# Optimization experiments

Measured on AMD Instinct MI355X. Metric: run time of the kernel, lower is better.

## Reference

```python
import jax, jax.numpy as jnp
import numpy as np

B, N, K = 32, 1024, 20

def _knn_idx(x, k):
    # x: [B, N, C] -> indices of k nearest neighbors (excluding self): [B, N, k]
    sq = jnp.sum(x * x, axis=-1)                      # [B, N]
    d = sq[:, :, None] + sq[:, None, :] - 2.0 * jnp.einsum('bnc,bmc->bnm', x, x)
    d = jnp.where(jnp.eye(x.shape[1], dtype=bool)[None], jnp.inf, d)
    _, idx = jax.lax.top_k(-d, k)                     # smallest distances
    return idx

def _edge_conv(x, k, mlp):
    # x: [B, N, C]; dynamic kNN graph + nn(cat[x_i, x_j - x_i]) + max over neighbors
    idx = _knn_idx(x, k)                              # [B, N, k]
    xj = jax.vmap(lambda xb, ib: xb[ib])(x, idx)      # [B, N, k, C]
    xi = jnp.broadcast_to(x[:, :, None, :], xj.shape)
    msg = mlp(jnp.concatenate([xi, xj - xi], axis=-1))  # [B, N, k, H]
    return jnp.max(msg, axis=2)                       # [B, N, H]

def setup_inputs() -> dict:
    key = jax.random.key(0)
    ks = jax.random.split(key, 16)
    def lin(kk, fi, fo):
        return jax.random.normal(kk, (fi, fo), dtype=jnp.float32) / np.sqrt(fi)
    x = jax.random.normal(ks[0], (B * N, 3), dtype=jnp.float32)
    batch = jnp.repeat(jnp.arange(B, dtype=jnp.int64), N)
    return {
        'x': x, 'batch': batch,
        'W1': lin(ks[1], 6, 64),   'b1': jnp.zeros((64,), jnp.float32),
        'W2': lin(ks[2], 64, 64),  'b2': jnp.zeros((64,), jnp.float32),
        'W3': lin(ks[3], 64, 64),  'b3': jnp.zeros((64,), jnp.float32),
        'W4': lin(ks[4], 128, 128),'b4': jnp.zeros((128,), jnp.float32),
        'Wp': lin(ks[5], 128, 512),'bp': jnp.zeros((512,), jnp.float32),
        'Wt1': lin(ks[6], 512, 256),'bt1': jnp.zeros((256,), jnp.float32),
        'Wt2': lin(ks[7], 256, 40), 'bt2': jnp.zeros((40,), jnp.float32),
    }

def reference(x, batch, W1, b1, W2, b2, W3, b3, W4, b4, Wp, bp, Wt1, bt1, Wt2, bt2):
    xb = x.reshape(B, N, -1)  # equal-sized clouds per batch vector
    mlp1 = lambda h: jax.nn.relu(jax.nn.relu(jax.nn.relu(h @ W1 + b1) @ W2 + b2) @ W3 + b3)
    mlp2 = lambda h: jax.nn.relu(h @ W4 + b4)
    out = _edge_conv(xb, K, mlp1)          # [B, N, 64]
    out = _edge_conv(out, K, mlp2)         # [B, N, 128]
    out = jax.nn.relu(out @ Wp + bp)       # [B, N, 512]
    out = jnp.max(out, axis=1)             # global max pool -> [B, 512]
    out = jax.nn.relu(out @ Wt1 + bt1) @ Wt2 + bt2  # [B, 40]
    return out
```

## Files before the change

kernel.cpp:

```cpp
#include <hip/hip_runtime.h>
#include <math.h>

#define BN   1024
#define NB   32
#define KNN  20
#define NROWS (NB*BN)

typedef __attribute__((ext_vector_type(8))) short bf16x8_t;
typedef __attribute__((ext_vector_type(4))) float f32x4_t;

__device__ __forceinline__ float finf() { return __builtin_huge_valf(); }

__device__ __forceinline__ unsigned short f2bf(float f) {
  union { float f; unsigned u; } v; v.f = f;
  unsigned r = v.u + 0x7FFFu + ((v.u >> 16) & 1u);
  return (unsigned short)(r >> 16);
}
__device__ __forceinline__ float bf2f(unsigned short h) {
  union { unsigned u; float f; } v; v.u = ((unsigned)h) << 16; return v.f;
}

__device__ __forceinline__ unsigned fkey(float d) {
  union { float f; unsigned u; } v; v.f = d;
  return (v.u & 0x80000000u) ? ~v.u : (v.u | 0x80000000u);
}

__device__ __forceinline__ void emit20(const unsigned (&kq)[16], unsigned thr,
                                       int lane, unsigned short* __restrict__ idx_out) {
  const unsigned long long lmask = (1ull << lane) - 1ull;
  int base = 0;
#pragma unroll
  for (int t = 0; t < 16; ++t) {
    const bool ok = (kq[t] <= thr);
    const unsigned long long m = __ballot(ok);
    if (ok) idx_out[base + (int)__popcll(m & lmask)] = (unsigned short)(kq[t] & 1023u);
    base += (int)__popcll(m);
  }
}

__device__ __forceinline__ void emit20c(const unsigned (&kq)[16], unsigned P, int cnt_lt,
                                        int lane, unsigned short* __restrict__ idx_out) {
  const unsigned long long lmask = (1ull << lane) - 1ull;
  const int need = KNN - cnt_lt;
  int base_lt = 0, base_eq = 0;
#pragma unroll
  for (int t = 0; t < 16; ++t) {
    const bool lt = (kq[t] < P);
    const bool eq = ((kq[t] - P) < 1024u);
    const unsigned long long mlt = __ballot(lt);
    const unsigned long long meq = __ballot(eq);
    if (lt) idx_out[base_lt + (int)__popcll(mlt & lmask)] = (unsigned short)(kq[t] & 1023u);
    const int erank = base_eq + (int)__popcll(meq & lmask);
    if (eq && erank < need) idx_out[cnt_lt + erank] = (unsigned short)(kq[t] & 1023u);
    base_lt += (int)__popcll(mlt);
    base_eq += (int)__popcll(meq);
  }
}

__device__ __forceinline__ void select20x2(const unsigned (&k0)[16], const unsigned (&k1)[16],
    int lane, unsigned short* __restrict__ o0, unsigned short* __restrict__ o1) {
  unsigned p0 = 0u, p1 = 0u;
  bool d0 = false, d1 = false;
#pragma unroll 1
  for (int b = 31; b >= 10; --b) {
    if (!d0) {
      const unsigned cand = p0 | (1u << b);
      int cnt = 0;
#pragma unroll
      for (int t = 0; t < 16; ++t) cnt += (int)__popcll(__ballot(k0[t] < cand));
      if (cnt == KNN)      { p0 = cand - 1u; d0 = true; }
      else if (cnt < KNN)  { p0 = cand; }
    }
    if (!d1) {
      const unsigned cand = p1 | (1u << b);
      int cnt = 0;
#pragma unroll
      for (int t = 0; t < 16; ++t) cnt += (int)__popcll(__ballot(k1[t] < cand));
      if (cnt == KNN)      { p1 = cand - 1u; d1 = true; }
      else if (cnt < KNN)  { p1 = cand; }
    }
    if (d0 && d1) break;
  }
  if (d0) emit20(k0, p0, lane, o0);
  else {
    int c = 0;
#pragma unroll
    for (int t = 0; t < 16; ++t) c += (int)__popcll(__ballot(k0[t] < p0));
    emit20c(k0, p0, c, lane, o0);
  }
  if (d1) emit20(k1, p1, lane, o1);
  else {
    int c = 0;
#pragma unroll
    for (int t = 0; t < 16; ++t) c += (int)__popcll(__ballot(k1[t] < p1));
    emit20c(k1, p1, c, lane, o1);
  }
}

__global__ __launch_bounds__(256) void prep_kernel(const float* __restrict__ W2, const float* __restrict__ W3,
    const float* __restrict__ W4, const float* __restrict__ Wp,
    unsigned short* __restrict__ w2b, unsigned short* __restrict__ w3b,
    unsigned short* __restrict__ w4b, unsigned short* __restrict__ wpb) {
  const int i = blockIdx.x * 256 + threadIdx.x;
  if (i < 512) {
    const int lane = i & 63, ks = (i >> 6) & 1, nt = i >> 7;
    const int col = nt*16 + (lane & 15), k0 = ks*32 + ((lane >> 4) << 3);
#pragma unroll
    for (int e = 0; e < 8; ++e) w2b[i*8 + e] = f2bf(W2[(size_t)(k0 + e)*64 + col]);
  } else if (i < 1024) {
    const int ii = i - 512;
    const int lane = ii & 63, ks = (ii >> 6) & 1, nt = ii >> 7;
    const int col = nt*16 + (lane & 15), k0 = ks*32 + ((lane >> 4) << 3);
#pragma unroll
    for (int e = 0; e < 8; ++e) w3b[ii*8 + e] = f2bf(W3[(size_t)(k0 + e)*64 + col]);
  } else if (i < 3072) {
    const int ii = i - 1024;
    const int lane = ii & 63, ks = (ii >> 6) & 3, nt = ii >> 8;
    const int col = nt*16 + (lane & 15), k0 = ks*32 + ((lane >> 4) << 3);
#pragma unroll
    for (int e = 0; e < 8; ++e) w4b[ii*8 + e] = f2bf(W4[(size_t)(k0 + e)*128 + col]);
  } else if (i < 11264) {
    const int ii = i - 3072;
    const int lane = ii & 63, ks = (ii >> 6) & 3, nt = ii >> 8;
    const int col = nt*16 + (lane & 15), k0 = ks*32 + ((lane >> 4) << 3);
#pragma unroll
    for (int e = 0; e < 8; ++e) {
      const float v = Wp[(size_t)(k0 + e)*512 + col];
      const unsigned short h = f2bf(v);
      wpb[ii*8 + e]         = h;
      wpb[65536 + ii*8 + e] = f2bf(v - bf2f(h));
    }
  }
}

__global__ __launch_bounds__(256) void knn3_kernel(const float* __restrict__ x, unsigned short* __restrict__ idxo) {
  const int pair = blockIdx.x * 4 + (threadIdx.x >> 6);
  const int lane = threadIdx.x & 63;
  const int row0 = pair * 2;
  const int b = row0 >> 10;
  const int ia = row0 & (BN - 1), ib = ia + 1;
  const float* xb = x + (size_t)b * BN * 3;
  const float xa0 = xb[ia*3+0], xa1 = xb[ia*3+1], xa2 = xb[ia*3+2];
  const float xb0 = xb[ib*3+0], xb1 = xb[ib*3+1], xb2 = xb[ib*3+2];
  const float sqa = xa0*xa0 + xa1*xa1 + xa2*xa2;
  const float sqb = xb0*xb0 + xb1*xb1 + xb2*xb2;
  unsigned k0[16], k1[16];
#pragma unroll
  for (int t = 0; t < 16; ++t) {
    const int j = (t << 6) | lane;
    const float a0 = xb[j*3+0], a1 = xb[j*3+1], a2 = xb[j*3+2];
    const float sqj = a0*a0 + a1*a1 + a2*a2;
    const float da  = sqa + sqj - 2.0f*(xa0*a0 + xa1*a1 + xa2*a2);
    const float db  = sqb + sqj - 2.0f*(xb0*a0 + xb1*a1 + xb2*a2);
    k0[t] = (j == ia) ? 0xFFFFFFFFu : ((fkey(da) & 0xFFFFFC00u) | (unsigned)j);
    k1[t] = (j == ib) ? 0xFFFFFFFFu : ((fkey(db) & 0xFFFFFC00u) | (unsigned)j);
  }
  select20x2(k0, k1, lane, idxo + (size_t)row0 * KNN, idxo + (size_t)(row0 + 1) * KNN);
}

__global__ __launch_bounds__(256) void edge1_mfma_kernel(const float* __restrict__ x, const unsigned short* __restrict__ idx,
    const float* __restrict__ W1, const float* __restrict__ B1,
    const unsigned short* __restrict__ w2b, const float* __restrict__ B2,
    const unsigned short* __restrict__ w3b, const float* __restrict__ B3,
    float* __restrict__ out1, unsigned short* __restrict__ hib,
    unsigned short* __restrict__ lob, float* __restrict__ sqbuf) {
  __shared__ unsigned short Hs1[80*64];
  __shared__ unsigned short Hs2[80*64];
  __shared__ float part[4][4];
  const int t = threadIdx.x, lane = t & 63, w = t >> 6;
  const int node0 = blockIdx.x * 4;

  const int bcol = w*16 + (lane & 15);
  bf16x8_t Bf2[2], Bf3[2];
#pragma unroll
  for (int ks = 0; ks < 2; ++ks) {
    Bf2[ks] = *(const bf16x8_t*)&w2b[(size_t)((w*2 + ks)*64 + lane) * 8];
    Bf3[ks] = *(const bf16x8_t*)&w3b[(size_t)((w*2 + ks)*64 + lane) * 8];
  }

  float w1c[6];
#pragma unroll
  for (int c = 0; c < 6; ++c) w1c[c] = W1[c*64 + lane];
  const float b1o = B1[lane];
  for (int r = w; r < 80; r += 4) {
    const int g = (r * 205) >> 12;
    const int e = r - g*20;
    const int node = node0 + g;
    const int b = node >> 10;
    const int j = idx[(size_t)node*KNN + e];
    const float xi0 = x[(size_t)node*3+0], xi1 = x[(size_t)node*3+1], xi2 = x[(size_t)node*3+2];
    const size_t jr = ((size_t)(b*BN + j))*3;
    const float h3 = x[jr+0]-xi0, h4 = x[jr+1]-xi1, h5 = x[jr+2]-xi2;
    float z = b1o + xi0*w1c[0] + xi1*w1c[1] + xi2*w1c[2]
                  + h3*w1c[3] + h4*w1c[4] + h5*w1c[5];
    z = fmaxf(z, 0.0f);
    Hs1[r*64 + (((lane>>3) ^ (r&7))<<3) + (lane&7)] = f2bf(z);
  }
  __syncthreads();

  f32x4_t acc[5];
#pragma unroll
  for (int mt = 0; mt < 5; ++mt) acc[mt] = (f32x4_t){0,0,0,0};
#pragma unroll
  for (int ks = 0; ks < 2; ++ks) {
#pragma unroll
    for (int mt = 0; mt < 5; ++mt) {
      const int r = mt*16 + (lane & 15);
      const int chunk = ks*4 + (lane >> 4);
      const bf16x8_t a = *(const bf16x8_t*)&Hs1[r*64 + ((chunk ^ (r&7))<<3)];
      acc[mt] = __builtin_amdgcn_mfma_f32_16x16x32_bf16(a, Bf2[ks], acc[mt], 0,0,0);
    }
  }
  {
    const float b2o = B2[bcol];
    const int rbase = (lane >> 4) * 4;
#pragma unroll
    for (int mt = 0; mt < 5; ++mt) {
#pragma unroll
      for (int reg = 0; reg < 4; ++reg) {
        const int row = mt*16 + rbase + reg;
        const float v = fmaxf(acc[mt][reg] + b2o, 0.0f);
        Hs2[row*64 + (((bcol>>3) ^ (row&7))<<3) + (bcol&7)] = f2bf(v);
      }
    }
  }
  __syncthreads();

#pragma unroll
  for (int mt = 0; mt < 5; ++mt) acc[mt] = (f32x4_t){0,0,0,0};
#pragma unroll
  for (int ks = 0; ks < 2; ++ks) {
#pragma unroll
    for (int mt = 0; mt < 5; ++mt) {
      const int r = mt*16 + (lane & 15);
      const int chunk = ks*4 + (lane >> 4);
      const bf16x8_t a = *(const bf16x8_t*)&Hs2[r*64 + ((chunk ^ (r&7))<<3)];
      acc[mt] = __builtin_amdgcn_mfma_f32_16x16x32_bf16(a, Bf3[ks], acc[mt], 0,0,0);
    }
  }

  {
    const float b3o = B3[bcol];
    const int rbase = (lane >> 4) * 4;
    float nm0 = 0.0f, nm1 = 0.0f, nm2 = 0.0f, nm3 = 0.0f;
#pragma unroll
    for (int mt = 0; mt < 5; ++mt) {
#pragma unroll
      for (int reg = 0; reg < 4; ++reg) {
        const int r = mt*16 + rbase + reg;
        const int g = (r * 205) >> 12;
        const float v = fmaxf(acc[mt][reg] + b3o, 0.0f);
        nm0 = (g == 0) ? fmaxf(nm0, v) : nm0;
        nm1 = (g == 1) ? fmaxf(nm1, v) : nm1;
        nm2 = (g == 2) ? fmaxf(nm2, v) : nm2;
        nm3 = (g == 3) ? fmaxf(nm3, v) : nm3;
      }
    }
#pragma unroll
    for (int off = 16; off <= 32; off <<= 1) {
      nm0 = fmaxf(nm0, __shfl_xor(nm0, off, 64));
      nm1 = fmaxf(nm1, __shfl_xor(nm1, off, 64));
      nm2 = fmaxf(nm2, __shfl_xor(nm2, off, 64));
      nm3 = fmaxf(nm3, __shfl_xor(nm3, off, 64));
    }
    const int gq = lane >> 4;
    const float m = (gq == 0) ? nm0 : (gq == 1) ? nm1 : (gq == 2) ? nm2 : nm3;
    const int node = node0 + gq;
    out1[(size_t)node*64 + bcol] = m;
    const unsigned short h = f2bf(m);
    hib[(size_t)node*64 + bcol] = h;
    lob[(size_t)node*64 + bcol] = f2bf(m - bf2f(h));
    float s = m * m;
#pragma unroll
    for (int off = 1; off <= 8; off <<= 1) s += __shfl_xor(s, off, 64);
    if ((lane & 15) == 0) part[gq][w] = s;
  }
  __syncthreads();
  if (t < 4) sqbuf[node0 + t] = part[t][0] + part[t][1] + part[t][2] + part[t][3];
}

__global__ __launch_bounds__(512) void knn64_mfma_kernel(
    const unsigned short* __restrict__ hi, const unsigned short* __restrict__ lo,
    const float* __restrict__ sq, unsigned short* __restrict__ idxo) {
  __shared__ unsigned Dmat[16 * 1024];
  const int t = threadIdx.x, lane = t & 63, w = t >> 6;
  const int i0  = blockIdx.x * 16;
  const int b   = i0 >> 10;
  const int i0l = i0 & (BN - 1);

  const size_t arow = (size_t)(i0 + (lane & 15)) * 64;
  const int    koff = (lane >> 4) * 8;
  bf16x8_t Ahi[2], Alo[2];
#pragma unroll
  for (int ks = 0; ks < 2; ++ks) {
    Ahi[ks] = *(const bf16x8_t*)&hi[arow + ks*32 + koff];
    Alo[ks] = *(const bf16x8_t*)&lo[arow + ks*32 + koff];
  }

  f32x4_t acc[8];
#pragma unroll
  for (int nt = 0; nt < 8; ++nt) {
    const int jl = (8*w + nt)*16 + (lane & 15);
    const size_t jrow = ((size_t)(b << 10) + jl) * 64;
    const bf16x8_t Bhi0 = *(const bf16x8_t*)&hi[jrow + koff];
    const bf16x8_t Bhi1 = *(const bf16x8_t*)&hi[jrow + 32 + koff];
    const bf16x8_t Blo0 = *(const bf16x8_t*)&lo[jrow + koff];
    const bf16x8_t Blo1 = *(const bf16x8_t*)&lo[jrow + 32 + koff];
    f32x4_t a = (f32x4_t){0,0,0,0};
    a = __builtin_amdgcn_mfma_f32_16x16x32_bf16(Ahi[0], Bhi0, a, 0,0,0);
    a = __builtin_amdgcn_mfma_f32_16x16x32_bf16(Ahi[1], Bhi1, a, 0,0,0);
    a = __builtin_amdgcn_mfma_f32_16x16x32_bf16(Ahi[0], Blo0, a, 0,0,0);
    a = __builtin_amdgcn_mfma_f32_16x16x32_bf16(Ahi[1], Blo1, a, 0,0,0);
    a = __builtin_amdgcn_mfma_f32_16x16x32_bf16(Alo[0], Bhi0, a, 0,0,0);
    a = __builtin_amdgcn_mfma_f32_16x16x32_bf16(Alo[1], Bhi1, a, 0,0,0);
    acc[nt] = a;
  }

  const int rbase = (lane >> 4) * 4;
  float sqr[4];
#pragma unroll
  for (int r = 0; r < 4; ++r) sqr[r] = sq[i0 + rbase + r];
#pragma unroll
  for (int nt = 0; nt < 8; ++nt) {
    const int jl = (8*w + nt)*16 + (lane & 15);
    const float sqj = sq[(b << 10) + jl];
#pragma unroll
    for (int r = 0; r < 4; ++r) {
      const float d = sqr[r] + sqj - 2.0f * acc[nt][r];
      const unsigned kq = (jl == i0l + rbase + r) ? 0xFFFFFFFFu
                        : ((fkey(d) & 0xFFFFFC00u) | (unsigned)jl);
      Dmat[(rbase + r)*1024 + jl] = kq;
    }
  }
  __syncthreads();

  const int r0 = 2*w, r1 = 2*w + 1;
  unsigned k0[16], k1[16];
#pragma unroll
  for (int tt = 0; tt < 16; ++tt) {
    k0[tt] = Dmat[r0*1024 + tt*64 + lane];
    k1[tt] = Dmat[r1*1024 + tt*64 + lane];
  }
  select20x2(k0, k1, lane, idxo + (size_t)(i0 + r0) * KNN, idxo + (size_t)(i0 + r1) * KNN);
}

__global__ __launch_bounds__(256) void edge2_mfma_kernel(const float* __restrict__ f, const unsigned short* __restrict__ idx,
    const unsigned short* __restrict__ w4b, const float* __restrict__ B4,
    unsigned short* __restrict__ o2hi, unsigned short* __restrict__ o2lo) {
  __shared__ unsigned short Hs[160*128];
  const int t = threadIdx.x, lane = t & 63, w = t >> 6;
  const int node0 = blockIdx.x * 8;

  bf16x8_t Bfrag[2][4];
#pragma unroll
  for (int nti = 0; nti < 2; ++nti)
#pragma unroll
    for (int ks = 0; ks < 4; ++ks)
      Bfrag[nti][ks] = *(const bf16x8_t*)&w4b[(size_t)(((2*w + nti)*4 + ks)*64 + lane) * 8];

  const int cq = (lane & 15) * 4;
  const int ch1 = cq >> 3, ch2 = 8 + (cq >> 3), sub = cq & 4;
#pragma unroll 2
  for (int i = 0; i < 10; ++i) {
    const int r = w*40 + i*4 + (lane >> 4);
    const int g = (r * 205) >> 12;
    const int e = r - g*20;
    const int node = node0 + g;
    const int b = node >> 10;
    const int j = idx[(size_t)node*KNN + e];
    const float4 xi = *(const float4*)&f[(size_t)node*64 + cq];
    const float4 xj = *(const float4*)&f[((size_t)(b*BN + j))*64 + cq];
    ushort4 hxi, hdf;
    hxi.x = f2bf(xi.x); hxi.y = f2bf(xi.y); hxi.z = f2bf(xi.z); hxi.w = f2bf(xi.w);
    hdf.x = f2bf(xj.x - xi.x); hdf.y = f2bf(xj.y - xi.y);
    hdf.z = f2bf(xj.z - xi.z); hdf.w = f2bf(xj.w - xi.w);
    *(ushort4*)&Hs[r*128 + ((ch1 ^ (r&7))<<3) + sub] = hxi;
    *(ushort4*)&Hs[r*128 + ((ch2 ^ (r&7))<<3) + sub] = hdf;
  }
  __syncthreads();

  f32x4_t acc[10][2];
#pragma unroll
  for (int mt = 0; mt < 10; ++mt) { acc[mt][0] = (f32x4_t){0,0,0,0}; acc[mt][1] = (f32x4_t){0,0,0,0}; }
#pragma unroll
  for (int ks = 0; ks < 4; ++ks) {
#pragma unroll
    for (int mt = 0; mt < 10; ++mt) {
      const int r = mt*16 + (lane & 15);
      const int chunk = ks*4 + (lane >> 4);
      const bf16x8_t a = *(const bf16x8_t*)&Hs[r*128 + ((chunk ^ (r&7))<<3)];
      acc[mt][0] = __builtin_amdgcn_mfma_f32_16x16x32_bf16(a, Bfrag[0][ks], acc[mt][0], 0,0,0);
      acc[mt][1] = __builtin_amdgcn_mfma_f32_16x16x32_bf16(a, Bfrag[1][ks], acc[mt][1], 0,0,0);
    }
  }

  const float bb0 = B4[(2*w+0)*16 + (lane & 15)];
  const float bb1 = B4[(2*w+1)*16 + (lane & 15)];
  const int rbase = (lane >> 4) * 4;
  float nm[8][2];
#pragma unroll
  for (int g = 0; g < 8; ++g) { nm[g][0] = 0.0f; nm[g][1] = 0.0f; }
#pragma unroll
  for (int mt = 0; mt < 10; ++mt) {
#pragma unroll
    for (int reg = 0; reg < 4; ++reg) {
      const int base = mt*16 + reg;
      const int glo = base / 20, ghi = (base + 12) / 20;
      const int r = base + rbase;
      const float v0 = fmaxf(acc[mt][0][reg] + bb0, 0.0f);
      const float v1 = fmaxf(acc[mt][1][reg] + bb1, 0.0f);
      if (glo == ghi) {
        nm[glo][0] = fmaxf(nm[glo][0], v0);
        nm[glo][1] = fmaxf(nm[glo][1], v1);
      } else {
        const bool hi = (r >= ghi*20);
        nm[glo][0] = hi ? nm[glo][0] : fmaxf(nm[glo][0], v0);
        nm[glo][1] = hi ? nm[glo][1] : fmaxf(nm[glo][1], v1);
        nm[ghi][0] = hi ? fmaxf(nm[ghi][0], v0) : nm[ghi][0];
        nm[ghi][1] = hi ? fmaxf(nm[ghi][1], v1) : nm[ghi][1];
      }
    }
  }
#pragma unroll
  for (int off = 16; off <= 32; off <<= 1)
#pragma unroll
    for (int g = 0; g < 8; ++g) {
      nm[g][0] = fmaxf(nm[g][0], __shfl_xor(nm[g][0], off, 64));
      nm[g][1] = fmaxf(nm[g][1], __shfl_xor(nm[g][1], off, 64));
    }
  const int gq = lane >> 4;
#pragma unroll
  for (int g = 0; g < 8; ++g) {
    if ((g & 3) == gq) {
#pragma unroll
      for (int nti = 0; nti < 2; ++nti) {
        const float m = nm[g][nti];
        const size_t o = (size_t)(node0 + g)*128 + (2*w + nti)*16 + (lane & 15);
        const unsigned short h = f2bf(m);
        o2hi[o] = h;
        o2lo[o] = f2bf(m - bf2f(h));
      }
    }
  }
}

__global__ __launch_bounds__(512) void pool_mfma_kernel(const unsigned short* __restrict__ o2hi,
    const unsigned short* __restrict__ o2lo, const unsigned short* __restrict__ wpb,
    const float* __restrict__ bp, float* __restrict__ pooled) {
  const int t = threadIdx.x, lane = t & 63, w = t >> 6;
  const int b = blockIdx.x >> 3, chunk = blockIdx.x & 7;
  const int row0 = b*BN + chunk*128;
  const int koff = (lane >> 4) * 8;
  bf16x8_t Bhi[4][4], Blo[4][4];
#pragma unroll
  for (int q = 0; q < 4; ++q)
#pragma unroll
    for (int ks = 0; ks < 4; ++ks) {
      const int nt = w*4 + q;
      Bhi[q][ks] = *(const bf16x8_t*)&wpb[(size_t)((nt*4 + ks)*64 + lane) * 8];
      Blo[q][ks] = *(const bf16x8_t*)&wpb[65536 + (size_t)((nt*4 + ks)*64 + lane) * 8];
    }
  float colmax[4] = {-finf(), -finf(), -finf(), -finf()};
#pragma unroll 2
  for (int mt = 0; mt < 8; ++mt) {
    const size_t ar = (size_t)(row0 + mt*16 + (lane & 15)) * 128;
    bf16x8_t Ahi[4], Alo[4];
#pragma unroll
    for (int ks = 0; ks < 4; ++ks) {
      Ahi[ks] = *(const bf16x8_t*)&o2hi[ar + ks*32 + koff];
      Alo[ks] = *(const bf16x8_t*)&o2lo[ar + ks*32 + koff];
    }
#pragma unroll
    for (int q = 0; q < 4; ++q) {
      f32x4_t a = (f32x4_t){0,0,0,0};
#pragma unroll
      for (int ks = 0; ks < 4; ++ks) {
        a = __builtin_amdgcn_mfma_f32_16x16x32_bf16(Ahi[ks], Bhi[q][ks], a, 0,0,0);
        a = __builtin_amdgcn_mfma_f32_16x16x32_bf16(Ahi[ks], Blo[q][ks], a, 0,0,0);
        a = __builtin_amdgcn_mfma_f32_16x16x32_bf16(Alo[ks], Bhi[q][ks], a, 0,0,0);
      }
#pragma unroll
      for (int reg = 0; reg < 4; ++reg) colmax[q] = fmaxf(colmax[q], a[reg]);
    }
  }
#pragma unroll
  for (int off = 16; off <= 32; off <<= 1)
#pragma unroll
    for (int q = 0; q < 4; ++q) colmax[q] = fmaxf(colmax[q], __shfl_xor(colmax[q], off, 64));
  if (lane < 16) {
#pragma unroll
    for (int q = 0; q < 4; ++q) {
      const int col = (w*4 + q)*16 + lane;
      const float m = fmaxf(colmax[q] + bp[col], 0.0f);
      atomicMax((int*)(pooled + (size_t)b*512 + col), __float_as_int(m));
    }
  }
}

__global__ __launch_bounds__(256) void head_kernel(const float* __restrict__ pooled,
    const float* __restrict__ Wt1, const float* __restrict__ bt1,
    const float* __restrict__ Wt2, const float* __restrict__ bt2,
    float* __restrict__ out) {
  __shared__ float psh[512];
  __shared__ float h1sh[256];
  const int t = threadIdx.x, b = blockIdx.x;
  psh[t]       = pooled[(size_t)b*512 + t];
  psh[t + 256] = pooled[(size_t)b*512 + t + 256];
  __syncthreads();
  float z = bt1[t];
  for (int j = 0; j < 512; ++j) z += psh[j] * Wt1[(size_t)j*256 + t];
  h1sh[t] = fmaxf(z, 0.0f);
  __syncthreads();
  if (t < 40) {
    float z2 = bt2[t];
    for (int j = 0; j < 256; ++j) z2 += h1sh[j] * Wt2[(size_t)j*40 + t];
    out[(size_t)b*40 + t] = z2;
  }
}

extern "C" void kernel_launch(void* const* d_in, const int* in_sizes, int n_in,
                              void* d_out, int out_size, void* d_ws, size_t ws_size,
                              hipStream_t stream) {
  const float* x   = (const float*)d_in[0];
  const float* W1  = (const float*)d_in[2];
  const float* B1  = (const float*)d_in[3];
  const float* W2  = (const float*)d_in[4];
  const float* B2  = (const float*)d_in[5];
  const float* W3  = (const float*)d_in[6];
  const float* B3  = (const float*)d_in[7];
  const float* W4  = (const float*)d_in[8];
  const float* B4  = (const float*)d_in[9];
  const float* Wp  = (const float*)d_in[10];
  const float* bp  = (const float*)d_in[11];
  const float* Wt1 = (const float*)d_in[12];
  const float* bt1 = (const float*)d_in[13];
  const float* Wt2 = (const float*)d_in[14];
  const float* bt2 = (const float*)d_in[15];
  float* out = (float*)d_out;

  char* ws = (char*)d_ws;
  const size_t OFF_SQ     = 0;
  const size_t OFF_IDX1   = 131072;
  const size_t OFF_OUT1   = 1441792;
  const size_t OFF_IDX2   = 9830400;
  const size_t OFF_X      = 11141120;
  const size_t OFF_POOLED = 27918336;
  const size_t OFF_W2B    = 27983872;
  const size_t OFF_W3B    = 27992064;
  const size_t OFF_W4B    = 28000256;
  const size_t OFF_WPB    = 28033024;
  const size_t WS_NEEDED  = 28295168;
  if (ws_size < WS_NEEDED) return;

  float*          sqbuf  = (float*)(ws + OFF_SQ);
  unsigned short* idx1   = (unsigned short*)(ws + OFF_IDX1);
  float*          out1   = (float*)(ws + OFF_OUT1);
  unsigned short* idx2   = (unsigned short*)(ws + OFF_IDX2);
  unsigned short* hib    = (unsigned short*)(ws + OFF_X);
  unsigned short* lob    = (unsigned short*)(ws + OFF_X + 4194304);
  unsigned short* o2hi   = (unsigned short*)(ws + OFF_X);
  unsigned short* o2lo   = (unsigned short*)(ws + OFF_X + 8388608);
  float*          pooled = (float*)(ws + OFF_POOLED);
  unsigned short* w2b    = (unsigned short*)(ws + OFF_W2B);
  unsigned short* w3b    = (unsigned short*)(ws + OFF_W3B);
  unsigned short* w4b    = (unsigned short*)(ws + OFF_W4B);
  unsigned short* wpb    = (unsigned short*)(ws + OFF_WPB);

  prep_kernel      <<<44,          256, 0, stream>>>(W2, W3, W4, Wp, w2b, w3b, w4b, wpb);
  knn3_kernel      <<<NROWS/8,     256, 0, stream>>>(x, idx1);
  edge1_mfma_kernel<<<NROWS/4,     256, 0, stream>>>(x, idx1, W1, B1, w2b, B2, w3b, B3,
                                                     out1, hib, lob, sqbuf);
  knn64_mfma_kernel<<<NROWS/16,    512, 0, stream>>>(hib, lob, sqbuf, idx2);
  edge2_mfma_kernel<<<NROWS/8,     256, 0, stream>>>(out1, idx2, w4b, B4, o2hi, o2lo);
  hipMemsetAsync(pooled, 0, NB*512*sizeof(float), stream);
  pool_mfma_kernel <<<NB*8,        512, 0, stream>>>(o2hi, o2lo, wpb, bp, pooled);
  head_kernel      <<<NB,          256, 0, stream>>>(pooled, Wt1, bt1, Wt2, bt2, out);
}
```

Measured before the change: 372.2 us.

## Fuse second kNN and edge-conv2 into one kernel, drop fp32 out1 buffer

Merges the 64-dim kNN kernel with the second edge-conv kernel. The kNN indices now stay in shared memory, and the Dmat LDS buffer is reused as the edge feature tile. Edge1 no longer writes the fp32 out1 feature map; edge2 rebuilds x_i and x_j from the hi/lo bf16 pair instead. This removes one launch, the idx2 round trip and an 8MB fp32 write/read. The cost is that each block now runs two sequential halves with one output tile per wave, which may lower MFMA occupancy and adds extra syncs.

```diff
diff --git a/kernel.cpp b/kernel.cpp
--- a/kernel.cpp
+++ b/kernel.cpp
@@ -162,8 +162,8 @@
     const float* __restrict__ W1, const float* __restrict__ B1,
     const unsigned short* __restrict__ w2b, const float* __restrict__ B2,
     const unsigned short* __restrict__ w3b, const float* __restrict__ B3,
-    float* __restrict__ out1, unsigned short* __restrict__ hib,
-    unsigned short* __restrict__ lob, float* __restrict__ sqbuf) {
+    unsigned short* __restrict__ hib, unsigned short* __restrict__ lob,
+    float* __restrict__ sqbuf) {
   __shared__ unsigned short Hs1[80*64];
   __shared__ unsigned short Hs2[80*64];
   __shared__ float part[4][4];
@@ -266,7 +266,6 @@
     const int gq = lane >> 4;
     const float m = (gq == 0) ? nm0 : (gq == 1) ? nm1 : (gq == 2) ? nm2 : nm3;
     const int node = node0 + gq;
-    out1[(size_t)node*64 + bcol] = m;
     const unsigned short h = f2bf(m);
     hib[(size_t)node*64 + bcol] = h;
     lob[(size_t)node*64 + bcol] = f2bf(m - bf2f(h));
@@ -279,168 +278,164 @@
   if (t < 4) sqbuf[node0 + t] = part[t][0] + part[t][1] + part[t][2] + part[t][3];
 }
 
-__global__ __launch_bounds__(512) void knn64_mfma_kernel(
+__global__ __launch_bounds__(512) void knn64edge2_kernel(
     const unsigned short* __restrict__ hi, const unsigned short* __restrict__ lo,
-    const float* __restrict__ sq, unsigned short* __restrict__ idxo) {
+    const float* __restrict__ sq, const unsigned short* __restrict__ w4b,
+    const float* __restrict__ B4,
+    unsigned short* __restrict__ o2hi, unsigned short* __restrict__ o2lo) {
   __shared__ unsigned Dmat[16 * 1024];
+  __shared__ unsigned short idx_sh[16][KNN];
+  unsigned short* Hs = (unsigned short*)Dmat;
   const int t = threadIdx.x, lane = t & 63, w = t >> 6;
   const int i0  = blockIdx.x * 16;
   const int b   = i0 >> 10;
   const int i0l = i0 & (BN - 1);
 
-  const size_t arow = (size_t)(i0 + (lane & 15)) * 64;
-  const int    koff = (lane >> 4) * 8;
-  bf16x8_t Ahi[2], Alo[2];
-#pragma unroll
-  for (int ks = 0; ks < 2; ++ks) {
-    Ahi[ks] = *(const bf16x8_t*)&hi[arow + ks*32 + koff];
-    Alo[ks] = *(const bf16x8_t*)&lo[arow + ks*32 + koff];
-  }
-
-  f32x4_t acc[8];
-#pragma unroll
-  for (int nt = 0; nt < 8; ++nt) {
-    const int jl = (8*w + nt)*16 + (lane & 15);
-    const size_t jrow = ((size_t)(b << 10) + jl) * 64;
-    const bf16x8_t Bhi0 = *(const bf16x8_t*)&hi[jrow + koff];
-    const bf16x8_t Bhi1 = *(const bf16x8_t*)&hi[jrow + 32 + koff];
-    const bf16x8_t Blo0 = *(const bf16x8_t*)&lo[jrow + koff];
-    const bf16x8_t Blo1 = *(const bf16x8_t*)&lo[jrow + 32 + koff];
-    f32x4_t a = (f32x4_t){0,0,0,0};
-    a = __builtin_amdgcn_mfma_f32_16x16x32_bf16(Ahi[0], Bhi0, a, 0,0,0);
-    a = __builtin_amdgcn_mfma_f32_16x16x32_bf16(Ahi[1], Bhi1, a, 0,0,0);
-    a = __builtin_amdgcn_mfma_f32_16x16x32_bf16(Ahi[0], Blo0, a, 0,0,0);
-    a = __builtin_amdgcn_mfma_f32_16x16x32_bf16(Ahi[1], Blo1, a, 0,0,0);
-    a = __builtin_amdgcn_mfma_f32_16x16x32_bf16(Alo[0], Bhi0, a, 0,0,0);
-    a = __builtin_amdgcn_mfma_f32_16x16x32_bf16(Alo[1], Bhi1, a, 0,0,0);
-    acc[nt] = a;
-  }
-
-  const int rbase = (lane >> 4) * 4;
-  float sqr[4];
-#pragma unroll
-  for (int r = 0; r < 4; ++r) sqr[r] = sq[i0 + rbase + r];
-#pragma unroll
-  for (int nt = 0; nt < 8; ++nt) {
-    const int jl = (8*w + nt)*16 + (lane & 15);
-    const float sqj = sq[(b << 10) + jl];
-#pragma unroll
-    for (int r = 0; r < 4; ++r) {
-      const float d = sqr[r] + sqj - 2.0f * acc[nt][r];
-      const unsigned kq = (jl == i0l + rbase + r) ? 0xFFFFFFFFu
-                        : ((fkey(d) & 0xFFFFFC00u) | (unsigned)jl);
-      Dmat[(rbase + r)*1024 + jl] = kq;
-    }
-  }
-  __syncthreads();
-
-  const int r0 = 2*w, r1 = 2*w + 1;
-  unsigned k0[16], k1[16];
-#pragma unroll
-  for (int tt = 0; tt < 16; ++tt) {
-    k0[tt] = Dmat[r0*1024 + tt*64 + lane];
-    k1[tt] = Dmat[r1*1024 + tt*64 + lane];
-  }
-  select20x2(k0, k1, lane, idxo + (size_t)(i0 + r0) * KNN, idxo + (size_t)(i0 + r1) * KNN);
-}
-
-__global__ __launch_bounds__(256) void edge2_mfma_kernel(const float* __restrict__ f, const unsigned short* __restrict__ idx,
-    const unsigned short* __restrict__ w4b, const float* __restrict__ B4,
-    unsigned short* __restrict__ o2hi, unsigned short* __restrict__ o2lo) {
-  __shared__ unsigned short Hs[160*128];
-  const int t = threadIdx.x, lane = t & 63, w = t >> 6;
-  const int node0 = blockIdx.x * 8;
-
-  bf16x8_t Bfrag[2][4];
-#pragma unroll
-  for (int nti = 0; nti < 2; ++nti)
-#pragma unroll
-    for (int ks = 0; ks < 4; ++ks)
-      Bfrag[nti][ks] = *(const bf16x8_t*)&w4b[(size_t)(((2*w + nti)*4 + ks)*64 + lane) * 8];
-
+  {
+    const size_t arow = (size_t)(i0 + (lane & 15)) * 64;
+    const int    koff = (lane >> 4) * 8;
+    bf16x8_t Ahi[2], Alo[2];
+#pragma unroll
+    for (int ks = 0; ks < 2; ++ks) {
+      Ahi[ks] = *(const bf16x8_t*)&hi[arow + ks*32 + koff];
+      Alo[ks] = *(const bf16x8_t*)&lo[arow + ks*32 + koff];
+    }
+    f32x4_t acc[8];
+#pragma unroll
+    for (int nt = 0; nt < 8; ++nt) {
+      const int jl = (8*w + nt)*16 + (lane & 15);
+      const size_t jrow = ((size_t)(b << 10) + jl) * 64;
+      const bf16x8_t Bhi0 = *(const bf16x8_t*)&hi[jrow + koff];
+      const bf16x8_t Bhi1 = *(const bf16x8_t*)&hi[jrow + 32 + koff];
+      const bf16x8_t Blo0 = *(const bf16x8_t*)&lo[jrow + koff];
+      const bf16x8_t Blo1 = *(const bf16x8_t*)&lo[jrow + 32 + koff];
+      f32x4_t a = (f32x4_t){0,0,0,0};
+      a = __builtin_amdgcn_mfma_f32_16x16x32_bf16(Ahi[0], Bhi0, a, 0,0,0);
+      a = __builtin_amdgcn_mfma_f32_16x16x32_bf16(Ahi[1], Bhi1, a, 0,0,0);
+      a = __builtin_amdgcn_mfma_f32_16x16x32_bf16(Ahi[0], Blo0, a, 0,0,0);
+      a = __builtin_amdgcn_mfma_f32_16x16x32_bf16(Ahi[1], Blo1, a, 0,0,0);
+      a = __builtin_amdgcn_mfma_f32_16x16x32_bf16(Alo[0], Bhi0, a, 0,0,0);
+      a = __builtin_amdgcn_mfma_f32_16x16x32_bf16(Alo[1], Bhi1, a, 0,0,0);
+      acc[nt] = a;
+    }
+    const int rbase = (lane >> 4) * 4;
+    float sqr[4];
+#pragma unroll
+    for (int r = 0; r < 4; ++r) sqr[r] = sq[i0 + rbase + r];
+#pragma unroll
+    for (int nt = 0; nt < 8; ++nt) {
+      const int jl = (8*w + nt)*16 + (lane & 15);
+      const float sqj = sq[(b << 10) + jl];
+#pragma unroll
+      for (int r = 0; r < 4; ++r) {
+        const float d = sqr[r] + sqj - 2.0f * acc[nt][r];
+        const unsigned kq = (jl == i0l + rbase + r) ? 0xFFFFFFFFu
+                          : ((fkey(d) & 0xFFFFFC00u) | (unsigned)jl);
+        Dmat[(rbase + r)*1024 + jl] = kq;
+      }
+    }
+  }
+  __syncthreads();
+
+  {
+    const int r0 = 2*w, r1 = 2*w + 1;
+    unsigned k0[16], k1[16];
+#pragma unroll
+    for (int tt = 0; tt < 16; ++tt) {
+      k0[tt] = Dmat[r0*1024 + tt*64 + lane];
+      k1[tt] = Dmat[r1*1024 + tt*64 + lane];
+    }
+    select20x2(k0, k1, lane, &idx_sh[r0][0], &idx_sh[r1][0]);
+  }
+  __syncthreads();
+
+  bf16x8_t Bfrag[4];
+#pragma unroll
+  for (int ks = 0; ks < 4; ++ks)
+    Bfrag[ks] = *(const bf16x8_t*)&w4b[(size_t)((w*4 + ks)*64 + lane) * 8];
+  const float bb = B4[w*16 + (lane & 15)];
   const int cq = (lane & 15) * 4;
   const int ch1 = cq >> 3, ch2 = 8 + (cq >> 3), sub = cq & 4;
-#pragma unroll 2
-  for (int i = 0; i < 10; ++i) {
-    const int r = w*40 + i*4 + (lane >> 4);
-    const int g = (r * 205) >> 12;
-    const int e = r - g*20;
-    const int node = node0 + g;
-    const int b = node >> 10;
-    const int j = idx[(size_t)node*KNN + e];
-    const float4 xi = *(const float4*)&f[(size_t)node*64 + cq];
-    const float4 xj = *(const float4*)&f[((size_t)(b*BN + j))*64 + cq];
-    ushort4 hxi, hdf;
-    hxi.x = f2bf(xi.x); hxi.y = f2bf(xi.y); hxi.z = f2bf(xi.z); hxi.w = f2bf(xi.w);
-    hdf.x = f2bf(xj.x - xi.x); hdf.y = f2bf(xj.y - xi.y);
-    hdf.z = f2bf(xj.z - xi.z); hdf.w = f2bf(xj.w - xi.w);
-    *(ushort4*)&Hs[r*128 + ((ch1 ^ (r&7))<<3) + sub] = hxi;
-    *(ushort4*)&Hs[r*128 + ((ch2 ^ (r&7))<<3) + sub] = hdf;
-  }
-  __syncthreads();
-
-  f32x4_t acc[10][2];
-#pragma unroll
-  for (int mt = 0; mt < 10; ++mt) { acc[mt][0] = (f32x4_t){0,0,0,0}; acc[mt][1] = (f32x4_t){0,0,0,0}; }
-#pragma unroll
-  for (int ks = 0; ks < 4; ++ks) {
+  const int rbase = (lane >> 4) * 4;
+
+#pragma unroll 1
+  for (int h = 0; h < 2; ++h) {
+    const int mynode = i0 + h*8 + w;
+    const size_t noff = (size_t)mynode*64 + cq;
+    const ushort4 hxi = *(const ushort4*)&hi[noff];
+    const ushort4 lxi = *(const ushort4*)&lo[noff];
+    const float xi0 = bf2f(hxi.x) + bf2f(lxi.x);
+    const float xi1 = bf2f(hxi.y) + bf2f(lxi.y);
+    const float xi2 = bf2f(hxi.z) + bf2f(lxi.z);
+    const float xi3 = bf2f(hxi.w) + bf2f(lxi.w);
+#pragma unroll
+    for (int i = 0; i < 5; ++i) {
+      const int e = i*4 + (lane >> 4);
+      const int j = idx_sh[h*8 + w][e];
+      const size_t joff = ((size_t)(b*BN + j))*64 + cq;
+      const ushort4 hxj = *(const ushort4*)&hi[joff];
+      const ushort4 lxj = *(const ushort4*)&lo[joff];
+      ushort4 hdf;
+      hdf.x = f2bf(bf2f(hxj.x) + bf2f(lxj.x) - xi0);
+      hdf.y = f2bf(bf2f(hxj.y) + bf2f(lxj.y) - xi1);
+      hdf.z = f2bf(bf2f(hxj.z) + bf2f(lxj.z) - xi2);
+      hdf.w = f2bf(bf2f(hxj.w) + bf2f(lxj.w) - xi3);
+      const int r = w*20 + e;
+      *(ushort4*)&Hs[r*128 + ((ch1 ^ (r&7))<<3) + sub] = hxi;
+      *(ushort4*)&Hs[r*128 + ((ch2 ^ (r&7))<<3) + sub] = hdf;
+    }
+    __syncthreads();
+
+    f32x4_t acc2[10];
+#pragma unroll
+    for (int mt = 0; mt < 10; ++mt) acc2[mt] = (f32x4_t){0,0,0,0};
+#pragma unroll
+    for (int ks = 0; ks < 4; ++ks) {
+#pragma unroll
+      for (int mt = 0; mt < 10; ++mt) {
+        const int r = mt*16 + (lane & 15);
+        const int chunk = ks*4 + (lane >> 4);
+        const bf16x8_t a = *(const bf16x8_t*)&Hs[r*128 + ((chunk ^ (r&7))<<3)];
+        acc2[mt] = __builtin_amdgcn_mfma_f32_16x16x32_bf16(a, Bfrag[ks], acc2[mt], 0,0,0);
+      }
+    }
+
+    float nm[8];
+#pragma unroll
+    for (int g = 0; g < 8; ++g) nm[g] = 0.0f;
 #pragma unroll
     for (int mt = 0; mt < 10; ++mt) {
-      const int r = mt*16 + (lane & 15);
-      const int chunk = ks*4 + (lane >> 4);
-      const bf16x8_t a = *(const bf16x8_t*)&Hs[r*128 + ((chunk ^ (r&7))<<3)];
-      acc[mt][0] = __builtin_amdgcn_mfma_f32_16x16x32_bf16(a, Bfrag[0][ks], acc[mt][0], 0,0,0);
-      acc[mt][1] = __builtin_amdgcn_mfma_f32_16x16x32_bf16(a, Bfrag[1][ks], acc[mt][1], 0,0,0);
-    }
-  }
-
-  const float bb0 = B4[(2*w+0)*16 + (lane & 15)];
-  const float bb1 = B4[(2*w+1)*16 + (lane & 15)];
-  const int rbase = (lane >> 4) * 4;
-  float nm[8][2];
-#pragma unroll
-  for (int g = 0; g < 8; ++g) { nm[g][0] = 0.0f; nm[g][1] = 0.0f; }
-#pragma unroll
-  for (int mt = 0; mt < 10; ++mt) {
-#pragma unroll
-    for (int reg = 0; reg < 4; ++reg) {
-      const int base = mt*16 + reg;
-      const int glo = base / 20, ghi = (base + 12) / 20;
-      const int r = base + rbase;
-      const float v0 = fmaxf(acc[mt][0][reg] + bb0, 0.0f);
-      const float v1 = fmaxf(acc[mt][1][reg] + bb1, 0.0f);
-      if (glo == ghi) {
-        nm[glo][0] = fmaxf(nm[glo][0], v0);
-        nm[glo][1] = fmaxf(nm[glo][1], v1);
-      } else {
-        const bool hi = (r >= ghi*20);
-        nm[glo][0] = hi ? nm[glo][0] : fmaxf(nm[glo][0], v0);
-        nm[glo][1] = hi ? nm[glo][1] : fmaxf(nm[glo][1], v1);
-        nm[ghi][0] = hi ? fmaxf(nm[ghi][0], v0) : nm[ghi][0];
-        nm[ghi][1] = hi ? fmaxf(nm[ghi][1], v1) : nm[ghi][1];
-      }
-    }
-  }
-#pragma unroll
-  for (int off = 16; off <= 32; off <<= 1)
+#pragma unroll
+      for (int reg = 0; reg < 4; ++reg) {
+        const int base = mt*16 + reg;
+        const int glo = base / 20, ghi = (base + 12) / 20;
+        const int r = base + rbase;
+        const float v = fmaxf(acc2[mt][reg] + bb, 0.0f);
+        if (glo == ghi) {
+          nm[glo] = fmaxf(nm[glo], v);
+        } else {
+          const bool hi2 = (r >= ghi*20);
+          nm[glo] = hi2 ? nm[glo] : fmaxf(nm[glo], v);
+          nm[ghi] = hi2 ? fmaxf(nm[ghi], v) : nm[ghi];
+        }
+      }
+    }
+#pragma unroll
+    for (int off = 16; off <= 32; off <<= 1)
+#pragma unroll
+      for (int g = 0; g < 8; ++g) nm[g] = fmaxf(nm[g], __shfl_xor(nm[g], off, 64));
+    const int gq = lane >> 4;
 #pragma unroll
     for (int g = 0; g < 8; ++g) {
-      nm[g][0] = fmaxf(nm[g][0], __shfl_xor(nm[g][0], off, 64));
-      nm[g][1] = fmaxf(nm[g][1], __shfl_xor(nm[g][1], off, 64));
-    }
-  const int gq = lane >> 4;
-#pragma unroll
-  for (int g = 0; g < 8; ++g) {
-    if ((g & 3) == gq) {
-#pragma unroll
-      for (int nti = 0; nti < 2; ++nti) {
-        const float m = nm[g][nti];
-        const size_t o = (size_t)(node0 + g)*128 + (2*w + nti)*16 + (lane & 15);
-        const unsigned short h = f2bf(m);
-        o2hi[o] = h;
-        o2lo[o] = f2bf(m - bf2f(h));
-      }
-    }
+      if ((g & 3) == gq) {
+        const float m = nm[g];
+        const size_t o = (size_t)(i0 + h*8 + g)*128 + w*16 + (lane & 15);
+        const unsigned short hh = f2bf(m);
+        o2hi[o] = hh;
+        o2lo[o] = f2bf(m - bf2f(hh));
+      }
+    }
+    __syncthreads();
   }
 }
 
@@ -541,38 +536,36 @@
   char* ws = (char*)d_ws;
   const size_t OFF_SQ     = 0;
   const size_t OFF_IDX1   = 131072;
-  const size_t OFF_OUT1   = 1441792;
-  const size_t OFF_IDX2   = 9830400;
-  const size_t OFF_X      = 11141120;
-  const size_t OFF_POOLED = 27918336;
-  const size_t OFF_W2B    = 27983872;
-  const size_t OFF_W3B    = 27992064;
-  const size_t OFF_W4B    = 28000256;
-  const size_t OFF_WPB    = 28033024;
-  const size_t WS_NEEDED  = 28295168;
+  const size_t OFF_HIB    = 1441792;
+  const size_t OFF_LOB    = 5636096;
+  const size_t OFF_O2HI   = 9830400;
+  const size_t OFF_O2LO   = 18219008;
+  const size_t OFF_POOLED = 26607616;
+  const size_t OFF_W2B    = 26673152;
+  const size_t OFF_W3B    = 26681344;
+  const size_t OFF_W4B    = 26689536;
+  const size_t OFF_WPB    = 26722304;
+  const size_t WS_NEEDED  = 26984448;
   if (ws_size < WS_NEEDED) return;
 
   float*          sqbuf  = (float*)(ws + OFF_SQ);
   unsigned short* idx1   = (unsigned short*)(ws + OFF_IDX1);
-  float*          out1   = (float*)(ws + OFF_OUT1);
-  unsigned short* idx2   = (unsigned short*)(ws + OFF_IDX2);
-  unsigned short* hib    = (unsigned short*)(ws + OFF_X);
-  unsigned short* lob    = (unsigned short*)(ws + OFF_X + 4194304);
-  unsigned short* o2hi   = (unsigned short*)(ws + OFF_X);
-  unsigned short* o2lo   = (unsigned short*)(ws + OFF_X + 8388608);
+  unsigned short* hib    = (unsigned short*)(ws + OFF_HIB);
+  unsigned short* lob    = (unsigned short*)(ws + OFF_LOB);
+  unsigned short* o2hi   = (unsigned short*)(ws + OFF_O2HI);
+  unsigned short* o2lo   = (unsigned short*)(ws + OFF_O2LO);
   float*          pooled = (float*)(ws + OFF_POOLED);
   unsigned short* w2b    = (unsigned short*)(ws + OFF_W2B);
   unsigned short* w3b    = (unsigned short*)(ws + OFF_W3B);
   unsigned short* w4b    = (unsigned short*)(ws + OFF_W4B);
   unsigned short* wpb    = (unsigned short*)(ws + OFF_WPB);
 
-  prep_kernel      <<<44,          256, 0, stream>>>(W2, W3, W4, Wp, w2b, w3b, w4b, wpb);
-  knn3_kernel      <<<NROWS/8,     256, 0, stream>>>(x, idx1);
-  edge1_mfma_kernel<<<NROWS/4,     256, 0, stream>>>(x, idx1, W1, B1, w2b, B2, w3b, B3,
-                                                     out1, hib, lob, sqbuf);
-  knn64_mfma_kernel<<<NROWS/16,    512, 0, stream>>>(hib, lob, sqbuf, idx2);
-  edge2_mfma_kernel<<<NROWS/8,     256, 0, stream>>>(out1, idx2, w4b, B4, o2hi, o2lo);
+  prep_kernel       <<<44,          256, 0, stream>>>(W2, W3, W4, Wp, w2b, w3b, w4b, wpb);
+  knn3_kernel       <<<NROWS/8,     256, 0, stream>>>(x, idx1);
+  edge1_mfma_kernel <<<NROWS/4,     256, 0, stream>>>(x, idx1, W1, B1, w2b, B2, w3b, B3,
+                                                      hib, lob, sqbuf);
+  knn64edge2_kernel <<<NROWS/16,    512, 0, stream>>>(hib, lob, sqbuf, w4b, B4, o2hi, o2lo);
   hipMemsetAsync(pooled, 0, NB*512*sizeof(float), stream);
-  pool_mfma_kernel <<<NB*8,        512, 0, stream>>>(o2hi, o2lo, wpb, bp, pooled);
-  head_kernel      <<<NB,          256, 0, stream>>>(pooled, Wt1, bt1, Wt2, bt2, out);
-}
+  pool_mfma_kernel  <<<NB*8,        512, 0, stream>>>(o2hi, o2lo, wpb, bp, pooled);
+  head_kernel       <<<NB,          256, 0, stream>>>(pooled, Wt1, bt1, Wt2, bt2, out);
+}
```

Result: faster. 332.6 us (-10.6%).
